# Kernel optimization log

Measured on AMD Instinct MI355X. Metric: run time of the kernel, lower is better.

The kernel has to match this reference:

```python
import jax, jax.numpy as jnp
import numpy as np
from jax import lax

B, T_IN, D = 32, 512, 384
F = 384      # x_predictor_filter_size
K = 3        # kernel, padding=1 -> same length
LN_EPS = 1e-5


def setup_inputs() -> dict:
    key = jax.random.key(0)
    ks = jax.random.split(key, 8)
    s = 0.02
    return {
        "x": jax.random.normal(ks[0], (B, T_IN, D), dtype=jnp.float32),
        "target": jax.random.randint(ks[1], (B, T_IN), 0, 8, dtype=jnp.int32),
        "mel_max_length": 4096,
        "conv1_w": jax.random.normal(ks[2], (F, D, K), dtype=jnp.float32) * s,
        "conv1_b": jnp.zeros((F,), jnp.float32),
        "ln1_g": jnp.ones((F,), jnp.float32),
        "ln1_b": jnp.zeros((F,), jnp.float32),
        "conv2_w": jax.random.normal(ks[3], (F, F, K), dtype=jnp.float32) * s,
        "conv2_b": jnp.zeros((F,), jnp.float32),
        "ln2_g": jnp.ones((F,), jnp.float32),
        "ln2_b": jnp.zeros((F,), jnp.float32),
        "lin_w": jax.random.normal(ks[4], (F, 1), dtype=jnp.float32) * s,
        "lin_b": jnp.zeros((1,), jnp.float32),
    }


def _conv1d_same(h_ncl, w, b):
    # h_ncl: [B, C_in, T], w: [C_out, C_in, K], padding=1
    out = lax.conv_general_dilated(h_ncl, w, window_strides=(1,), padding=[(1, 1)],
                                   dimension_numbers=("NCH", "OIH", "NCH"))
    return out + b[None, :, None]


def _layernorm(h, g, b):
    mu = jnp.mean(h, axis=-1, keepdims=True)
    var = jnp.var(h, axis=-1, keepdims=True)
    return (h - mu) * lax.rsqrt(var + LN_EPS) * g + b


def _duration_predictor(x, conv1_w, conv1_b, ln1_g, ln1_b, conv2_w, conv2_b, ln2_g, ln2_b, lin_w, lin_b):
    h = _conv1d_same(jnp.transpose(x, (0, 2, 1)), conv1_w, conv1_b)       # [B,F,T]
    h = jax.nn.relu(_layernorm(jnp.transpose(h, (0, 2, 1)), ln1_g, ln1_b))  # [B,T,F]
    h = _conv1d_same(jnp.transpose(h, (0, 2, 1)), conv2_w, conv2_b)
    h = jax.nn.relu(_layernorm(jnp.transpose(h, (0, 2, 1)), ln2_g, ln2_b))
    return (h @ lin_w + lin_b)[..., 0]  # [B, T_in]


def _length_regulate(x, target, mel_max_length):
    # Equivalent to alignment @ x with one-hot alignment built by create_alignment,
    # expressed as a duration-indexed gather (same math, no dense [B,Tout,Tin]).
    ends = jnp.cumsum(target, axis=1)                 # [B, T_in]
    m = jnp.arange(mel_max_length)                    # [T_out]
    idx = jax.vmap(lambda e: jnp.searchsorted(e, m, side="right"))(ends)  # [B, T_out]
    valid = idx < target.shape[1]                     # frames past total duration -> zero pad
    idx = jnp.minimum(idx, target.shape[1] - 1)
    out = jnp.take_along_axis(x, idx[:, :, None], axis=1)  # [B, T_out, D]
    return out * valid[:, :, None].astype(x.dtype)


def reference(x, target, mel_max_length, conv1_w, conv1_b, ln1_g, ln1_b,
              conv2_w, conv2_b, ln2_g, ln2_b, lin_w, lin_b):
    dur_pred = _duration_predictor(x, conv1_w, conv1_b, ln1_g, ln1_b,
                                   conv2_w, conv2_b, ln2_g, ln2_b, lin_w, lin_b)
    output = _length_regulate(x, target, mel_max_length)
    return output, dur_pred
```

## Files before the change

kernel.cpp:

```cpp
#include <hip/hip_runtime.h>
#include <cstdint>
#include <cstddef>

#define B_   32
#define TIN  512
#define D_   384
#define F_   384
#define TOUT 4096
#define TPAD 514

typedef __bf16 bf16x8 __attribute__((ext_vector_type(8)));
typedef float  f32x4  __attribute__((ext_vector_type(4)));
typedef unsigned short u16x8 __attribute__((ext_vector_type(8)));

__device__ __forceinline__ unsigned short f2bf(float f) {
  unsigned int u = __float_as_uint(f);
  u += 0x7fff + ((u >> 16) & 1);
  return (unsigned short)(u >> 16);
}

__device__ __forceinline__ void load16_to_lds(const void* g, void* l) {
  __builtin_amdgcn_global_load_lds(
      (const __attribute__((address_space(1))) unsigned int*)g,
      (__attribute__((address_space(3))) unsigned int*)l, 16, 0, 0);
}

#define PB_CUM 32
#define PB_W   1152
#define PB_Z   96
#define PB_PX  3084
#define PB_TOT (PB_CUM + PB_W + PB_Z + PB_PX)

__global__ __launch_bounds__(256) void prep_all(
    const float* __restrict__ w1, const float* __restrict__ w2,
    unsigned short* __restrict__ Wt1, unsigned short* __restrict__ Wt2,
    unsigned short* __restrict__ h1p,
    const int* __restrict__ target, int* __restrict__ idxv,
    const float4* __restrict__ x4, unsigned short* __restrict__ xp) {
  int bx = blockIdx.x;
  int tid = threadIdx.x;

  if (bx < PB_CUM) {
    __shared__ int ends[512];
    __shared__ int ps[256];
    int b = bx;
    int a0 = target[b * TIN + 2 * tid];
    int a1 = target[b * TIN + 2 * tid + 1];
    ps[tid] = a0 + a1;
    __syncthreads();
    for (int off = 1; off < 256; off <<= 1) {
      int add = (tid >= off) ? ps[tid - off] : 0;
      __syncthreads();
      ps[tid] += add;
      __syncthreads();
    }
    int incl = ps[tid];
    ends[2 * tid + 1] = incl;
    ends[2 * tid]     = incl - a1;
    __syncthreads();
    for (int p = 0; p < 16; ++p) {
      int m = p * 256 + tid;
      int lo = 0, hi = 512;
      while (lo < hi) {
        int mid = (lo + hi) >> 1;
        if (ends[mid] <= m) lo = mid + 1; else hi = mid;
      }
      idxv[b * TOUT + m] = (lo < TIN) ? lo : -1;
    }
    return;
  }
  bx -= PB_CUM;

  if (bx < PB_W) {
    int g = bx * 256 + tid;
    const int FD = F_ * D_;
    int which = g >= FD;
    const float* w = which ? w2 : w1;
    unsigned short* o = which ? Wt2 : Wt1;
    int e = g - which * FD;
    o[e]          = f2bf(w[e * 3 + 0]);
    o[FD + e]     = f2bf(w[e * 3 + 1]);
    o[2 * FD + e] = f2bf(w[e * 3 + 2]);
    return;
  }
  bx -= PB_W;

  if (bx < PB_Z) {
    int z = bx * 256 + tid;
    int zr = z / D_;
    int c = z - zr * D_;
    int b = zr >> 1;
    int tp = (zr & 1) ? (TPAD - 1) : 0;
    h1p[((size_t)(b * TPAD + tp)) * D_ + c] = 0;
    return;
  }
  bx -= PB_Z;

  {
    int g = bx * 256 + tid;
    int row = g / 48;
    int c8 = g - row * 48;
    int b = row / TPAD;
    int tp = row - b * TPAD;
    u16x8 o;
    if (tp == 0 || tp == TPAD - 1) {
      o = (u16x8)0;
    } else {
      float4 v0 = x4[((size_t)(b * TIN + tp - 1)) * 96 + c8 * 2];
      float4 v1 = x4[((size_t)(b * TIN + tp - 1)) * 96 + c8 * 2 + 1];
      o[0] = f2bf(v0.x); o[1] = f2bf(v0.y); o[2] = f2bf(v0.z); o[3] = f2bf(v0.w);
      o[4] = f2bf(v1.x); o[5] = f2bf(v1.y); o[6] = f2bf(v1.z); o[7] = f2bf(v1.w);
    }
    *(u16x8*)(xp + (size_t)row * D_ + c8 * 8) = o;
  }
}

template <int MODE>
__global__ __launch_bounds__(512, 1) void conv_fused(
    const unsigned short* __restrict__ Ap, const unsigned short* __restrict__ Wt,
    const float* __restrict__ bias,
    const float* __restrict__ gam, const float* __restrict__ bet,
    const float* __restrict__ lw, const float* __restrict__ lb,
    unsigned short* __restrict__ hp, float* __restrict__ dur,
    const float4* __restrict__ x4, const int* __restrict__ idxv,
    float4* __restrict__ out4, int half) {
  __shared__ __align__(16) char smem[28672];
  unsigned short* As = (unsigned short*)smem;
  unsigned short* Bs = (unsigned short*)(smem + 4096);
  float* epi = (float*)smem;

  const int bx  = blockIdx.x;
  const int tid = threadIdx.x;
  const int cbq = bx / 3;

  if (bx - cbq * 3 != 0) {
    int gidx = bx - cbq - 1;
    size_t g = (size_t)half * 6291456 + (size_t)gidx * 512 + tid;
    for (int it = 0; it < 24; ++it, g += 262144) {
      unsigned int gu = (unsigned int)g;
      int fr = gu / 96;
      int c  = gu - fr * 96;
      int id = idxv[fr];
      int b  = fr >> 12;
      float4 v = {0.f, 0.f, 0.f, 0.f};
      if (id >= 0) v = x4[(size_t)(b * TIN + id) * 96 + c];
      out4[g] = v;
    }
    return;
  }

  const int wave = tid >> 6;
  const int lane = tid & 63;
  const int quad = lane >> 4;
  const int l15  = lane & 15;
  const int wn = wave * 48;
  const int m0 = cbq * 64;
  const int b  = m0 >> 9;
  const int t0 = m0 & 511;
  const int arow = tid >> 2;
  const int acol = (tid & 3) * 8;

  f32x4 acc[4][3];
  for (int i = 0; i < 4; ++i)
    for (int j = 0; j < 3; ++j)
      acc[i][j] = (f32x4){0.f, 0.f, 0.f, 0.f};

  for (int kc = 0; kc < 36; ++kc) {
    int kw = kc / 12;
    int d0 = (kc - kw * 12) * 32;
    if (tid < 256)
      load16_to_lds(Ap + (size_t)(b * TPAD + t0 + arow + kw) * D_ + d0 + acol,
                    (char*)As + wave * 1024);
    for (int r = 0; r < 3; ++r)
      load16_to_lds(Wt + (size_t)(kw * F_ + r * 128 + arow) * D_ + d0 + acol,
                    (char*)Bs + r * 8192 + wave * 1024);
    __syncthreads();
    bf16x8 av[4], bv[3];
    for (int mi = 0; mi < 4; ++mi)
      av[mi] = *(const bf16x8*)(As + (mi * 16 + l15) * 32 + quad * 8);
    for (int ni = 0; ni < 3; ++ni)
      bv[ni] = *(const bf16x8*)(Bs + (wn + ni * 16 + l15) * 32 + quad * 8);
    for (int mi = 0; mi < 4; ++mi)
      for (int ni = 0; ni < 3; ++ni)
        acc[mi][ni] = __builtin_amdgcn_mfma_f32_16x16x32_bf16(av[mi], bv[ni], acc[mi][ni], 0, 0, 0);
    __syncthreads();
  }

  float gv[6], bv2[6], lwv[6];
  for (int j = 0; j < 6; ++j) {
    int c = lane + j * 64;
    gv[j]  = gam[c];
    bv2[j] = bet[c];
    if (MODE == 1) lwv[j] = lw[c];
  }
  float bb[3];
  for (int ni = 0; ni < 3; ++ni) bb[ni] = bias[wn + ni * 16 + l15];

  for (int g4 = 0; g4 < 4; ++g4) {
    __syncthreads();
    for (int ni = 0; ni < 3; ++ni) {
      int c = wn + ni * 16 + l15;
      for (int r = 0; r < 4; ++r)
        epi[(quad * 4 + r) * 384 + c] = acc[g4][ni][r] + bb[ni];
    }
    __syncthreads();
    for (int rr = 0; rr < 2; ++rr) {
      int lr = wave * 2 + rr;
      int grow = m0 + g4 * 16 + lr;
      const float* p = epi + lr * 384;
      float v[6], s = 0.f, ss = 0.f;
      for (int j = 0; j < 6; ++j) {
        v[j] = p[lane + j * 64];
        s += v[j];
        ss += v[j] * v[j];
      }
      for (int off = 32; off; off >>= 1) {
        s  += __shfl_xor(s, off);
        ss += __shfl_xor(ss, off);
      }
      float mean = s * (1.f / 384.f);
      float var  = ss * (1.f / 384.f) - mean * mean;
      float rstd = rsqrtf(var + 1e-5f);
      if (MODE == 0) {
        unsigned short* o = hp + ((size_t)(b * TPAD + (grow & 511) + 1)) * D_;
        for (int j = 0; j < 6; ++j) {
          float y = (v[j] - mean) * rstd * gv[j] + bv2[j];
          y = y > 0.f ? y : 0.f;
          o[lane + j * 64] = f2bf(y);
        }
      } else {
        float a = 0.f;
        for (int j = 0; j < 6; ++j) {
          float y = (v[j] - mean) * rstd * gv[j] + bv2[j];
          y = y > 0.f ? y : 0.f;
          a += y * lwv[j];
        }
        for (int off = 32; off; off >>= 1) a += __shfl_xor(a, off);
        if (lane == 0) dur[grow] = a + lb[0];
      }
    }
  }
}

extern "C" void kernel_launch(void* const* d_in, const int* in_sizes, int n_in,
                              void* d_out, int out_size, void* d_ws, size_t ws_size,
                              hipStream_t stream) {
  const float* x      = (const float*)d_in[0];
  const int*   target = (const int*)d_in[1];
  const float* w1  = (const float*)d_in[3];
  const float* b1  = (const float*)d_in[4];
  const float* g1  = (const float*)d_in[5];
  const float* be1 = (const float*)d_in[6];
  const float* w2  = (const float*)d_in[7];
  const float* b2  = (const float*)d_in[8];
  const float* g2  = (const float*)d_in[9];
  const float* be2 = (const float*)d_in[10];
  const float* lw  = (const float*)d_in[11];
  const float* lb  = (const float*)d_in[12];

  float* out = (float*)d_out;
  float* dur = out + (size_t)B_ * TOUT * D_;

  char* ws = (char*)d_ws;
  unsigned short* xp   = (unsigned short*)(ws);
  unsigned short* h1p  = (unsigned short*)(ws + 12632064);
  unsigned short* Wt1  = (unsigned short*)(ws + 25264128);
  unsigned short* Wt2  = (unsigned short*)(ws + 26148864);
  int*            idxv = (int*)(ws + 27033600);

  prep_all<<<dim3(PB_TOT), dim3(256), 0, stream>>>(
      w1, w2, Wt1, Wt2, h1p, target, idxv, (const float4*)x, xp);
  conv_fused<0><<<dim3(768), dim3(512), 0, stream>>>(
      xp, Wt1, b1, g1, be1, nullptr, nullptr, h1p, nullptr,
      (const float4*)x, idxv, (float4*)out, 0);
  conv_fused<1><<<dim3(768), dim3(512), 0, stream>>>(
      h1p, Wt2, b2, g2, be2, lw, lb, nullptr, dur,
      (const float4*)x, idxv, (float4*)out, 1);
}
```

Baseline: 323.6 us.

## Stage padded activation tile in LDS once and stream weights from global

After: 359.8 us. +11.2%, slower.

```diff
diff --git a/kernel.cpp b/kernel.cpp
--- a/kernel.cpp
+++ b/kernel.cpp
@@ -7,7 +7,6 @@
 #define D_   384
 #define F_   384
 #define TOUT 4096
-#define TPAD 514
 
 typedef __bf16 bf16x8 __attribute__((ext_vector_type(8)));
 typedef float  f32x4  __attribute__((ext_vector_type(4)));
@@ -19,24 +18,14 @@
   return (unsigned short)(u >> 16);
 }
 
-__device__ __forceinline__ void load16_to_lds(const void* g, void* l) {
-  __builtin_amdgcn_global_load_lds(
-      (const __attribute__((address_space(1))) unsigned int*)g,
-      (__attribute__((address_space(3))) unsigned int*)l, 16, 0, 0);
-}
-
 #define PB_CUM 32
 #define PB_W   1152
-#define PB_Z   96
-#define PB_PX  3084
-#define PB_TOT (PB_CUM + PB_W + PB_Z + PB_PX)
+#define PB_TOT (PB_CUM + PB_W)
 
 __global__ __launch_bounds__(256) void prep_all(
     const float* __restrict__ w1, const float* __restrict__ w2,
     unsigned short* __restrict__ Wt1, unsigned short* __restrict__ Wt2,
-    unsigned short* __restrict__ h1p,
-    const int* __restrict__ target, int* __restrict__ idxv,
-    const float4* __restrict__ x4, unsigned short* __restrict__ xp) {
+    const int* __restrict__ target, int* __restrict__ idxv) {
   int bx = blockIdx.x;
   int tid = threadIdx.x;
 
@@ -71,7 +60,7 @@
   }
   bx -= PB_CUM;
 
-  if (bx < PB_W) {
+  {
     int g = bx * 256 + tid;
     const int FD = F_ * D_;
     int which = g >= FD;
@@ -81,53 +70,21 @@
     o[e]          = f2bf(w[e * 3 + 0]);
     o[FD + e]     = f2bf(w[e * 3 + 1]);
     o[2 * FD + e] = f2bf(w[e * 3 + 2]);
-    return;
-  }
-  bx -= PB_W;
-
-  if (bx < PB_Z) {
-    int z = bx * 256 + tid;
-    int zr = z / D_;
-    int c = z - zr * D_;
-    int b = zr >> 1;
-    int tp = (zr & 1) ? (TPAD - 1) : 0;
-    h1p[((size_t)(b * TPAD + tp)) * D_ + c] = 0;
-    return;
-  }
-  bx -= PB_Z;
-
-  {
-    int g = bx * 256 + tid;
-    int row = g / 48;
-    int c8 = g - row * 48;
-    int b = row / TPAD;
-    int tp = row - b * TPAD;
-    u16x8 o;
-    if (tp == 0 || tp == TPAD - 1) {
-      o = (u16x8)0;
-    } else {
-      float4 v0 = x4[((size_t)(b * TIN + tp - 1)) * 96 + c8 * 2];
-      float4 v1 = x4[((size_t)(b * TIN + tp - 1)) * 96 + c8 * 2 + 1];
-      o[0] = f2bf(v0.x); o[1] = f2bf(v0.y); o[2] = f2bf(v0.z); o[3] = f2bf(v0.w);
-      o[4] = f2bf(v1.x); o[5] = f2bf(v1.y); o[6] = f2bf(v1.z); o[7] = f2bf(v1.w);
-    }
-    *(u16x8*)(xp + (size_t)row * D_ + c8 * 8) = o;
   }
 }
 
 template <int MODE>
-__global__ __launch_bounds__(512, 1) void conv_fused(
-    const unsigned short* __restrict__ Ap, const unsigned short* __restrict__ Wt,
+__global__ __launch_bounds__(512, 4) void conv_fused(
+    const float* __restrict__ xin,
+    const unsigned short* __restrict__ hin,
+    const unsigned short* __restrict__ Wt,
     const float* __restrict__ bias,
     const float* __restrict__ gam, const float* __restrict__ bet,
     const float* __restrict__ lw, const float* __restrict__ lb,
-    unsigned short* __restrict__ hp, float* __restrict__ dur,
+    unsigned short* __restrict__ hout, float* __restrict__ dur,
     const float4* __restrict__ x4, const int* __restrict__ idxv,
     float4* __restrict__ out4, int half) {
-  __shared__ __align__(16) char smem[28672];
-  unsigned short* As = (unsigned short*)smem;
-  unsigned short* Bs = (unsigned short*)(smem + 4096);
-  float* epi = (float*)smem;
+  __shared__ __attribute__((aligned(16))) char smem[50688];
 
   const int bx  = blockIdx.x;
   const int tid = threadIdx.x;
@@ -135,16 +92,20 @@
 
   if (bx - cbq * 3 != 0) {
     int gidx = bx - cbq - 1;
-    size_t g = (size_t)half * 6291456 + (size_t)gidx * 512 + tid;
-    for (int it = 0; it < 24; ++it, g += 262144) {
-      unsigned int gu = (unsigned int)g;
-      int fr = gu / 96;
-      int c  = gu - fr * 96;
-      int id = idxv[fr];
-      int b  = fr >> 12;
+    int b  = half * 16 + (gidx >> 5);
+    int r0 = (gidx & 31) * 128;
+    const int* idxp = idxv + b * TOUT + r0;
+    const float4* xb = x4 + (size_t)b * (TIN * 96);
+    float4* ob = out4 + ((size_t)b * TOUT + r0) * 96;
+    #pragma unroll 8
+    for (int it = 0; it < 24; ++it) {
+      int j = it * 512 + tid;
+      int row = j / 96;
+      int c = j - row * 96;
+      int id = idxp[row];
       float4 v = {0.f, 0.f, 0.f, 0.f};
-      if (id >= 0) v = x4[(size_t)(b * TIN + id) * 96 + c];
-      out4[g] = v;
+      if (id >= 0) v = xb[id * 96 + c];
+      ob[j] = v;
     }
     return;
   }
@@ -153,64 +114,91 @@
   const int lane = tid & 63;
   const int quad = lane >> 4;
   const int l15  = lane & 15;
-  const int wn = wave * 48;
-  const int m0 = cbq * 64;
-  const int b  = m0 >> 9;
-  const int t0 = m0 & 511;
-  const int arow = tid >> 2;
-  const int acol = (tid & 3) * 8;
+  const int wn   = wave * 48;
+  const int m0   = cbq * 64;
+  const int b    = m0 >> 9;
+  const int t0   = m0 & 511;
+
+  for (int p = 0; p < 7; ++p) {
+    int ch = p * 512 + tid;
+    if (ch < 3168) {
+      int row = ch / 48;
+      int ci  = ch - row * 48;
+      int t   = t0 + row - 1;
+      u16x8 val;
+      if ((unsigned)t >= (unsigned)TIN) {
+        val = (u16x8)0;
+      } else if (MODE == 0) {
+        const float4* xr = (const float4*)xin + ((size_t)(b * TIN + t)) * 96 + ci * 2;
+        float4 v0 = xr[0], v1 = xr[1];
+        val[0] = f2bf(v0.x); val[1] = f2bf(v0.y); val[2] = f2bf(v0.z); val[3] = f2bf(v0.w);
+        val[4] = f2bf(v1.x); val[5] = f2bf(v1.y); val[6] = f2bf(v1.z); val[7] = f2bf(v1.w);
+      } else {
+        val = *(const u16x8*)(hin + ((size_t)(b * TIN + t)) * D_ + ci * 8);
+      }
+      unsigned int byte = ((unsigned int)(row * 768 + ci * 16)) ^ (((unsigned)row & 7u) << 4);
+      *(u16x8*)(smem + byte) = val;
+    }
+  }
+  __syncthreads();
 
   f32x4 acc[4][3];
   for (int i = 0; i < 4; ++i)
     for (int j = 0; j < 3; ++j)
       acc[i][j] = (f32x4){0.f, 0.f, 0.f, 0.f};
 
-  for (int kc = 0; kc < 36; ++kc) {
-    int kw = kc / 12;
-    int d0 = (kc - kw * 12) * 32;
-    if (tid < 256)
-      load16_to_lds(Ap + (size_t)(b * TPAD + t0 + arow + kw) * D_ + d0 + acol,
-                    (char*)As + wave * 1024);
-    for (int r = 0; r < 3; ++r)
-      load16_to_lds(Wt + (size_t)(kw * F_ + r * 128 + arow) * D_ + d0 + acol,
-                    (char*)Bs + r * 8192 + wave * 1024);
-    __syncthreads();
-    bf16x8 av[4], bv[3];
-    for (int mi = 0; mi < 4; ++mi)
-      av[mi] = *(const bf16x8*)(As + (mi * 16 + l15) * 32 + quad * 8);
-    for (int ni = 0; ni < 3; ++ni)
-      bv[ni] = *(const bf16x8*)(Bs + (wn + ni * 16 + l15) * 32 + quad * 8);
-    for (int mi = 0; mi < 4; ++mi)
+  const unsigned short* Bb = Wt + (size_t)(wn + l15) * D_ + quad * 8;
+
+  for (int kw = 0; kw < 3; ++kw) {
+    const unsigned short* Bk = Bb + kw * (F_ * D_);
+    const unsigned int rb = (unsigned int)((l15 + kw) * 768 + quad * 16);
+    const unsigned int sw = (((unsigned)(l15 + kw)) & 7u) << 4;
+    #pragma unroll 4
+    for (int dc = 0; dc < 12; ++dc) {
+      const int d0 = dc * 32;
+      bf16x8 bv[3], av[4];
       for (int ni = 0; ni < 3; ++ni)
-        acc[mi][ni] = __builtin_amdgcn_mfma_f32_16x16x32_bf16(av[mi], bv[ni], acc[mi][ni], 0, 0, 0);
-    __syncthreads();
-  }
-
-  float gv[6], bv2[6], lwv[6];
+        bv[ni] = *(const bf16x8*)(Bk + ni * (16 * D_) + d0);
+      for (int mi = 0; mi < 4; ++mi)
+        av[mi] = *(const bf16x8*)(smem + ((rb + mi * 12288 + d0 * 2) ^ sw));
+      for (int mi = 0; mi < 4; ++mi)
+        for (int ni = 0; ni < 3; ++ni)
+          acc[mi][ni] = __builtin_amdgcn_mfma_f32_16x16x32_bf16(av[mi], bv[ni], acc[mi][ni], 0, 0, 0);
+    }
+  }
+
+  float gvv[6], bvv[6], lwv[6];
   for (int j = 0; j < 6; ++j) {
     int c = lane + j * 64;
-    gv[j]  = gam[c];
-    bv2[j] = bet[c];
+    gvv[j] = gam[c];
+    bvv[j] = bet[c];
     if (MODE == 1) lwv[j] = lw[c];
   }
   float bb[3];
   for (int ni = 0; ni < 3; ++ni) bb[ni] = bias[wn + ni * 16 + l15];
 
-  for (int g4 = 0; g4 < 4; ++g4) {
-    __syncthreads();
-    for (int ni = 0; ni < 3; ++ni) {
-      int c = wn + ni * 16 + l15;
-      for (int r = 0; r < 4; ++r)
-        epi[(quad * 4 + r) * 384 + c] = acc[g4][ni][r] + bb[ni];
-    }
-    __syncthreads();
-    for (int rr = 0; rr < 2; ++rr) {
-      int lr = wave * 2 + rr;
-      int grow = m0 + g4 * 16 + lr;
-      const float* p = epi + lr * 384;
+  for (int g = 0; g < 2; ++g) {
+    __syncthreads();
+    for (int mi2 = 0; mi2 < 2; ++mi2) {
+      int mi = g * 2 + mi2;
+      for (int ni = 0; ni < 3; ++ni) {
+        int cc = wn + ni * 16 + l15;
+        for (int r = 0; r < 4; ++r) {
+          int wr = mi2 * 16 + quad * 4 + r;
+          unsigned int byte = ((unsigned int)(wr * 1536 + cc * 4)) ^ ((((unsigned)wr >> 2) & 3u) << 4);
+          *(float*)(smem + byte) = acc[mi][ni][r] + bb[ni];
+        }
+      }
+    }
+    __syncthreads();
+    for (int rr = 0; rr < 4; ++rr) {
+      int lr = wave * 4 + rr;
+      int grow = m0 + g * 32 + lr;
+      unsigned int swr = (((unsigned)lr >> 2) & 3u) << 4;
       float v[6], s = 0.f, ss = 0.f;
       for (int j = 0; j < 6; ++j) {
-        v[j] = p[lane + j * 64];
+        unsigned int byte = ((unsigned int)(lr * 1536 + (lane + j * 64) * 4)) ^ swr;
+        v[j] = *(const float*)(smem + byte);
         s += v[j];
         ss += v[j] * v[j];
       }
@@ -222,16 +210,16 @@
       float var  = ss * (1.f / 384.f) - mean * mean;
       float rstd = rsqrtf(var + 1e-5f);
       if (MODE == 0) {
-        unsigned short* o = hp + ((size_t)(b * TPAD + (grow & 511) + 1)) * D_;
+        unsigned short* o = hout + ((size_t)(b * TIN + (grow & 511))) * D_;
         for (int j = 0; j < 6; ++j) {
-          float y = (v[j] - mean) * rstd * gv[j] + bv2[j];
+          float y = (v[j] - mean) * rstd * gvv[j] + bvv[j];
           y = y > 0.f ? y : 0.f;
           o[lane + j * 64] = f2bf(y);
         }
       } else {
         float a = 0.f;
         for (int j = 0; j < 6; ++j) {
-          float y = (v[j] - mean) * rstd * gv[j] + bv2[j];
+          float y = (v[j] - mean) * rstd * gvv[j] + bvv[j];
           y = y > 0.f ? y : 0.f;
           a += y * lwv[j];
         }
@@ -262,18 +250,17 @@
   float* dur = out + (size_t)B_ * TOUT * D_;
 
   char* ws = (char*)d_ws;
-  unsigned short* xp   = (unsigned short*)(ws);
-  unsigned short* h1p  = (unsigned short*)(ws + 12632064);
-  unsigned short* Wt1  = (unsigned short*)(ws + 25264128);
-  unsigned short* Wt2  = (unsigned short*)(ws + 26148864);
-  int*            idxv = (int*)(ws + 27033600);
+  unsigned short* h1   = (unsigned short*)(ws);
+  unsigned short* Wt1  = (unsigned short*)(ws + 12582912);
+  unsigned short* Wt2  = (unsigned short*)(ws + 13467648);
+  int*            idxv = (int*)(ws + 14352384);
 
   prep_all<<<dim3(PB_TOT), dim3(256), 0, stream>>>(
-      w1, w2, Wt1, Wt2, h1p, target, idxv, (const float4*)x, xp);
+      w1, w2, Wt1, Wt2, target, idxv);
   conv_fused<0><<<dim3(768), dim3(512), 0, stream>>>(
-      xp, Wt1, b1, g1, be1, nullptr, nullptr, h1p, nullptr,
-      (const float4*)x, idxv, (float4*)out, 0);
+      x, nullptr, Wt1, b1, g1, be1, nullptr, nullptr,
+      h1, nullptr, (const float4*)x, idxv, (float4*)out, 0);
   conv_fused<1><<<dim3(768), dim3(512), 0, stream>>>(
-      h1p, Wt2, b2, g2, be2, lw, lb, nullptr, dur,
-      (const float4*)x, idxv, (float4*)out, 1);
-}
+      nullptr, h1, Wt2, b2, g2, be2, lw, lb,
+      nullptr, dur, (const float4*)x, idxv, (float4*)out, 1);
+}
```
